# Performance work log

Hardware: AMD Instinct MI355X
Metric: run time of the kernel (lower is better)

## Reference

```python
import jax, jax.numpy as jnp
import numpy as np
from jax import lax

SIGMA = 5
RADIUS = int(4 * SIGMA + 0.5)  # 20 -> kernel size 41, pad_size = 41//2 = 20 = RADIUS
D_AP = 2.27
D_DV = 2.27


def _gauss_d1_kernel():
    # gaussian_kernel1d(sigma, order=1, radius): q(x) = -x/sigma^2, kernel = q(x)*phi(x)
    x = np.arange(-RADIUS, RADIUS + 1).astype(np.float64)
    phi = np.exp(-0.5 / SIGMA ** 2 * x ** 2)
    phi = phi / phi.sum()
    return ((-x / SIGMA ** 2) * phi).astype(np.float32)

_KERNEL = jnp.asarray(_gauss_d1_kernel())


def _conv1d_valid(x, k):
    # x: [N, L], k: [K] -> [N, L-K+1]; cross-correlation, same as torch F.conv1d
    return lax.conv_general_dilated(x[:, None, :], k[None, None, :], (1,), 'VALID')[:, 0, :]


def diffY(x):
    # circular padding along H, derivative / dDV
    c, h, w = x.shape
    xp = jnp.pad(x, ((0, 0), (RADIUS, RADIUS), (0, 0)), mode='wrap')
    xp = jnp.transpose(xp, (0, 2, 1)).reshape(c * w, h + 2 * RADIUS)
    out = _conv1d_valid(xp, _KERNEL).reshape(c, w, h)
    return jnp.transpose(out, (0, 2, 1)) / D_DV


def diffX(x):
    # reflect padding along W, derivative / dAP
    c, h, w = x.shape
    xp = jnp.pad(x, ((0, 0), (0, 0), (RADIUS, RADIUS)), mode='reflect')
    out = _conv1d_valid(xp.reshape(c * h, w + 2 * RADIUS), _KERNEL).reshape(c, h, w)
    return out / D_AP


def setup_inputs() -> dict:
    key = jax.random.key(0)
    k1, k2, k3, k4, k5 = jax.random.split(key, 5)
    H, W = 1024, 2048
    return {
        'y': jax.random.normal(k1, (5, H, W), dtype=jnp.float32),
        'v': jax.random.normal(k2, (2, H, W), dtype=jnp.float32),
        'gamma_ds': jax.random.normal(k3, (H, W), dtype=jnp.float32),
        'cad_coefs': jax.random.uniform(k4, (3,), dtype=jnp.float32),
        'myo_coefs': jax.random.uniform(k5, (5,), dtype=jnp.float32),
    }


def reference(y, v, gamma_ds, cad_coefs, myo_coefs):
    H, W = y.shape[-2:]
    m4 = y[:4]                                  # [4,H,W] myosin components
    c1 = y[4:]                                  # [1,H,W] cadherin

    d1_m = jnp.stack([diffY(m4), diffX(m4)], axis=-1).reshape(2, 2, H, W, 2)
    m = m4.reshape(2, 2, H, W)
    d1_c = jnp.stack([diffY(c1), diffX(c1)], axis=-1).reshape(H, W, 2)
    c = c1[0]

    d1_v = jnp.stack([diffY(v), diffX(v)], axis=-1)   # [2,H,W,2]: d1_v[i,y,x,j] = d_j v_i
    gv = jnp.einsum('iyxj->ijyx', d1_v)
    gvT = jnp.einsum('jyxi->ijyx', d1_v)
    O = -0.5 * (gv - gvT)                       # vorticity
    E = 0.5 * (gv + gvT)                        # strain rate

    eye = jnp.eye(2, dtype=y.dtype)[:, :, None, None]
    trm_yx = jnp.einsum('kkyx->yx', m)
    deviatoric = m - 0.5 * trm_yx[None, None] * eye

    m_norm = jnp.sqrt(jnp.sum(m * m, axis=(0, 1), keepdims=True))            # [1,1,H,W]
    m_0 = jnp.mean(m_norm, axis=(2, 3), keepdims=True)                       # [1,1,1,1]
    dev_mag = jnp.sqrt(jnp.sum(deviatoric * deviatoric, axis=(0, 1), keepdims=True))
    devE = jnp.einsum('klyx,klyx->yx', deviatoric, E)[None, None]

    E_active = E - jnp.sign(devE) * devE * deviatoric / dev_mag ** 2
    E_active = 0.5 * E_active * dev_mag / m_0
    E_passive = E - E_active

    mE = (jnp.einsum('ikyx,kjyx->ijyx', m, E_passive)
          + jnp.einsum('ikyx,kjyx->ijyx', E_passive, m))

    cad = jax.nn.relu(cad_coefs)
    myo = jax.nn.relu(myo_coefs)

    cdot = (-jnp.einsum('iyx,yxi->yx', v, d1_c)
            - cad[0] * c
            + cad[1] * c * jnp.einsum('iyxi->yx', d1_v)
            + cad[2] * gamma_ds)

    trm = trm_yx[None, None]
    gamma_dv = jnp.array([[1.0, 0.0], [0.0, 0.0]], dtype=y.dtype)[:, :, None, None]

    mdot = (-jnp.einsum('kyx,ijyxk->ijyx', v, d1_m)
            - jnp.einsum('ikyx,kjyx->ijyx', O, m)
            + jnp.einsum('ikyx,kjyx->ijyx', m, O)
            - myo[0] * m
            + myo[1] * mE
            - myo[2] * c[None, None] * mE
            + myo[3] * trm * gamma_dv
            + myo[4] * trm * m)

    return jnp.concatenate([mdot.reshape(4, H, W), cdot[None]], axis=0)
```

## Files before the change

kernel.cpp:

```cpp
#include <hip/hip_runtime.h>
#include <math.h>

#define RAD 20
#define KLEN 41
#define NH 1024
#define NW 2048
#define NHW (NH * NW)

struct KW { float w[KLEN]; };
constexpr double cexp_neg(double u) {
  double term = 1.0, sum = 1.0;
  for (int k = 1; k < 30; ++k) { term *= (-u) / (double)k; sum += term; }
  return sum;
}
constexpr KW make_kw() {
  KW r{};
  double ph[KLEN] = {};
  double s = 0.0;
  for (int i = 0; i < KLEN; ++i) {
    double d = (double)(i - RAD);
    double e = cexp_neg(d * d / 800.0);
    e = e * e; e = e * e; e = e * e; e = e * e;
    ph[i] = e; s += e;
  }
  for (int i = 0; i < KLEN; ++i) {
    double d = (double)(i - RAD);
    r.w[i] = (float)((-d / 25.0) * (ph[i] / s) / 2.27);
  }
  return r;
}
static constexpr KW KWC = make_kw();

template <int K>
__device__ __forceinline__ void tap(float s, float& r0, float& r1, float& r2,
                                    float& r3, float& r4, float& r5, float& r6,
                                    float& r7) {
  if constexpr (K - 0 >= 0 && K - 0 <= 40) r0 = fmaf(s, KWC.w[K - 0], r0);
  if constexpr (K - 1 >= 0 && K - 1 <= 40) r1 = fmaf(s, KWC.w[K - 1], r1);
  if constexpr (K - 2 >= 0 && K - 2 <= 40) r2 = fmaf(s, KWC.w[K - 2], r2);
  if constexpr (K - 3 >= 0 && K - 3 <= 40) r3 = fmaf(s, KWC.w[K - 3], r3);
  if constexpr (K - 4 >= 0 && K - 4 <= 40) r4 = fmaf(s, KWC.w[K - 4], r4);
  if constexpr (K - 5 >= 0 && K - 5 <= 40) r5 = fmaf(s, KWC.w[K - 5], r5);
  if constexpr (K - 6 >= 0 && K - 6 <= 40) r6 = fmaf(s, KWC.w[K - 6], r6);
  if constexpr (K - 7 >= 0 && K - 7 <= 40) r7 = fmaf(s, KWC.w[K - 7], r7);
}

#define R8 r0, r1, r2, r3, r4, r5, r6, r7

#define TW 64
#define TH 32
#define TILE_CH ((TH + 2 * RAD) * TW)

__device__ __forceinline__ void conv_col(const float* __restrict__ t, int base,
                                         int lane, float& r0, float& r1,
                                         float& r2, float& r3, float& r4,
                                         float& r5, float& r6, float& r7) {
#define CCHUNK(c)                                      \
  {                                                    \
    float s0 = t[(base + 4 * (c) + 0) * TW + lane];    \
    float s1 = t[(base + 4 * (c) + 1) * TW + lane];    \
    float s2 = t[(base + 4 * (c) + 2) * TW + lane];    \
    float s3 = t[(base + 4 * (c) + 3) * TW + lane];    \
    tap<4 * (c) + 0>(s0, R8);                          \
    tap<4 * (c) + 1>(s1, R8);                          \
    tap<4 * (c) + 2>(s2, R8);                          \
    tap<4 * (c) + 3>(s3, R8);                          \
  }
  CCHUNK(0) CCHUNK(1) CCHUNK(2) CCHUNK(3) CCHUNK(4) CCHUNK(5)
  CCHUNK(6) CCHUNK(7) CCHUNK(8) CCHUNK(9) CCHUNK(10) CCHUNK(11)
#undef CCHUNK
}

__global__ __launch_bounds__(256) void k_reduce(const float* __restrict__ y,
                                                double* __restrict__ acc) {
  const int tid = blockIdx.x * blockDim.x + threadIdx.x;
  const int stride = gridDim.x * blockDim.x;
  double local = 0.0;
  for (int q = tid; q < NHW / 4; q += stride) {
    float4 a = ((const float4*)y)[q];
    float4 b = ((const float4*)(y + NHW))[q];
    float4 c = ((const float4*)(y + 2 * (size_t)NHW))[q];
    float4 d = ((const float4*)(y + 3 * (size_t)NHW))[q];
    local += (double)sqrtf(a.x * a.x + b.x * b.x + c.x * c.x + d.x * d.x);
    local += (double)sqrtf(a.y * a.y + b.y * b.y + c.y * c.y + d.y * d.y);
    local += (double)sqrtf(a.z * a.z + b.z * b.z + c.z * c.z + d.z * d.z);
    local += (double)sqrtf(a.w * a.w + b.w * b.w + c.w * c.w + d.w * d.w);
  }
#pragma unroll
  for (int off = 32; off > 0; off >>= 1) local += __shfl_down(local, off, 64);
  __shared__ double smem[4];
  const int lane = threadIdx.x & 63;
  const int wid = threadIdx.x >> 6;
  if (lane == 0) smem[wid] = local;
  __syncthreads();
  if (threadIdx.x == 0) {
    double s = smem[0] + smem[1] + smem[2] + smem[3];
    atomicAdd(acc, s);
  }
}

__global__ __launch_bounds__(256) void k_dx(const float* __restrict__ y,
                                            const float* __restrict__ v,
                                            float* __restrict__ ws) {
  __shared__ float row[2120];
  const int t = threadIdx.x;
  const int r = blockIdx.x;
  const int ch = blockIdx.y;
  const float* src = (ch < 5) ? (y + (size_t)ch * NHW) : (v + (size_t)(ch - 5) * NHW);
  const float* rp = src + (size_t)r * NW;

#define SWZ(i) ((i) + ((i) >> 6))
#define ST(i, val) { const int ii_ = (i); row[SWZ(ii_)] = (val); }

  const float4* rp4 = (const float4*)rp;
  float4 b0 = rp4[t];
  float4 b1 = rp4[t + 256];
  ST(RAD + 4 * t + 0, b0.x)
  ST(RAD + 4 * t + 1, b0.y)
  ST(RAD + 4 * t + 2, b0.z)
  ST(RAD + 4 * t + 3, b0.w)
  ST(RAD + 4 * (t + 256) + 0, b1.x)
  ST(RAD + 4 * (t + 256) + 1, b1.y)
  ST(RAD + 4 * (t + 256) + 2, b1.z)
  ST(RAD + 4 * (t + 256) + 3, b1.w)
  if (t < RAD) {
    ST(t, rp[RAD - t])
    ST(NW + RAD + t, rp[NW - 2 - t])
  }
  __syncthreads();

  const int xb = 8 * t;
  float r0 = 0.f, r1 = 0.f, r2 = 0.f, r3 = 0.f;
  float r4 = 0.f, r5 = 0.f, r6 = 0.f, r7 = 0.f;
#define RD(k) { const int x_ = xb + (k); float s_ = row[SWZ(x_)]; tap<(k)>(s_, R8); }
  RD(0)  RD(1)  RD(2)  RD(3)  RD(4)  RD(5)  RD(6)  RD(7)
  RD(8)  RD(9)  RD(10) RD(11) RD(12) RD(13) RD(14) RD(15)
  RD(16) RD(17) RD(18) RD(19) RD(20) RD(21) RD(22) RD(23)
  RD(24) RD(25) RD(26) RD(27) RD(28) RD(29) RD(30) RD(31)
  RD(32) RD(33) RD(34) RD(35) RD(36) RD(37) RD(38) RD(39)
  RD(40) RD(41) RD(42) RD(43) RD(44) RD(45) RD(46) RD(47)
#undef RD

  float4 o0, o1;
  o0.x = r0; o0.y = r1; o0.z = r2; o0.w = r3;
  o1.x = r4; o1.y = r5; o1.z = r6; o1.w = r7;
  float4* dst = (float4*)(ws + (size_t)(7 + ch) * NHW + (size_t)r * NW + xb);
  dst[0] = o0;
  dst[1] = o1;
}

__global__ __launch_bounds__(256, 4) void k_dyf(
    const float* __restrict__ y, const float* __restrict__ v,
    const float* __restrict__ gds, const float* __restrict__ cadc,
    const float* __restrict__ myoc, const float* __restrict__ ws,
    const double* __restrict__ acc, float* __restrict__ out) {
  __shared__ float tile[2 * TILE_CH];
  const int lane = threadIdx.x & 63;
  const int wid = threadIdx.x >> 6;
  const int x0 = blockIdx.x * TW;
  const int yb = blockIdx.y * TH;
  const int base = wid * 8;

  const float m0 = (float)(acc[0] / (double)NHW);
  const float cad0 = fmaxf(cadc[0], 0.f);
  const float cad1 = fmaxf(cadc[1], 0.f);
  const float cad2 = fmaxf(cadc[2], 0.f);
  const float my0 = fmaxf(myoc[0], 0.f);
  const float my1 = fmaxf(myoc[1], 0.f);
  const float my2 = fmaxf(myoc[2], 0.f);
  const float my3 = fmaxf(myoc[3], 0.f);
  const float my4 = fmaxf(myoc[4], 0.f);

#define GLL(g, k, srcp)                                                        \
  {                                                                            \
    const float* sp_ = (srcp) +                                                \
        (size_t)(((yb - RAD + wid + 4 * (k)) + NH) & (NH - 1)) * NW + x0 +     \
        lane;                                                                  \
    __builtin_amdgcn_global_load_lds(                                          \
        (const __attribute__((address_space(1))) void*)sp_,                    \
        (__attribute__((address_space(3))) void*)&tile[(g)*TILE_CH +           \
                                                       (wid + 4 * (k)) * TW],  \
        4, 0, 0);                                                              \
  }
#define STAGECH(g, srcp)                                                 \
  GLL(g, 0, srcp) GLL(g, 1, srcp) GLL(g, 2, srcp) GLL(g, 3, srcp)        \
  GLL(g, 4, srcp) GLL(g, 5, srcp) GLL(g, 6, srcp) GLL(g, 7, srcp)        \
  GLL(g, 8, srcp) GLL(g, 9, srcp) GLL(g, 10, srcp) GLL(g, 11, srcp)     \
  GLL(g, 12, srcp) GLL(g, 13, srcp) GLL(g, 14, srcp) GLL(g, 15, srcp)   \
  GLL(g, 16, srcp) GLL(g, 17, srcp)

#define DECL8(P)                                                       \
  float P##0 = 0.f, P##1 = 0.f, P##2 = 0.f, P##3 = 0.f, P##4 = 0.f,    \
        P##5 = 0.f, P##6 = 0.f, P##7 = 0.f;
#define CALLCONV(g, P)                                                  \
  conv_col(&tile[(g) * TILE_CH], base, lane, P##0, P##1, P##2, P##3,    \
           P##4, P##5, P##6, P##7);

  DECL8(ym00) DECL8(ym01) DECL8(ym10) DECL8(ym11)
  DECL8(yc) DECL8(yv0) DECL8(yv1)

  STAGECH(0, y)
  __syncthreads();
  STAGECH(1, y + (size_t)NHW)
  CALLCONV(0, ym00)
  __syncthreads();
  STAGECH(0, y + 2 * (size_t)NHW)
  CALLCONV(1, ym01)
  __syncthreads();
  STAGECH(1, y + 3 * (size_t)NHW)
  CALLCONV(0, ym10)
  __syncthreads();
  STAGECH(0, y + 4 * (size_t)NHW)
  CALLCONV(1, ym11)
  __syncthreads();
  STAGECH(1, v)
  CALLCONV(0, yc)
  __syncthreads();
  STAGECH(0, v + (size_t)NHW)
  CALLCONV(1, yv0)
  __syncthreads();
  CALLCONV(0, yv1)

#define POINT(q)                                                              \
  {                                                                           \
    const size_t idx = (size_t)(yb + base + (q)) * NW + x0 + lane;            \
    const float m00 = y[idx];                                                 \
    const float m01 = y[idx + (size_t)NHW];                                   \
    const float m10 = y[idx + 2 * (size_t)NHW];                               \
    const float m11 = y[idx + 3 * (size_t)NHW];                               \
    const float c = y[idx + 4 * (size_t)NHW];                                 \
    const float v0 = v[idx];                                                  \
    const float v1 = v[idx + (size_t)NHW];                                    \
    const float g = gds[idx];                                                 \
    const float dY_m00 = ym00##q, dY_m01 = ym01##q;                           \
    const float dY_m10 = ym10##q, dY_m11 = ym11##q;                           \
    const float dY_c = yc##q, dY_v0 = yv0##q, dY_v1 = yv1##q;                 \
    const float dX_m00 = ws[idx + 7 * (size_t)NHW];                           \
    const float dX_m01 = ws[idx + 8 * (size_t)NHW];                           \
    const float dX_m10 = ws[idx + 9 * (size_t)NHW];                           \
    const float dX_m11 = ws[idx + 10 * (size_t)NHW];                          \
    const float dX_c = ws[idx + 11 * (size_t)NHW];                            \
    const float dX_v0 = ws[idx + 12 * (size_t)NHW];                           \
    const float dX_v1 = ws[idx + 13 * (size_t)NHW];                           \
    const float gv00 = dY_v0, gv01 = dX_v0, gv10 = dY_v1, gv11 = dX_v1;       \
    const float ww = -0.5f * (gv01 - gv10);                                   \
    const float E00 = gv00, E11 = gv11;                                       \
    const float E01 = 0.5f * (gv01 + gv10);                                   \
    const float E10 = E01;                                                    \
    const float trm = m00 + m11;                                              \
    const float dev00 = m00 - 0.5f * trm;                                     \
    const float dev01 = m01;                                                  \
    const float dev10 = m10;                                                  \
    const float dev11 = m11 - 0.5f * trm;                                     \
    const float dmag_sq =                                                     \
        dev00 * dev00 + dev01 * dev01 + dev10 * dev10 + dev11 * dev11;        \
    const float dm = sqrtf(dmag_sq);                                          \
    const float dm2 = dm * dm;                                                \
    const float devE = dev00 * E00 + dev01 * E01 + dev10 * E10 + dev11 * E11; \
    const float sg = (devE > 0.f) ? 1.f : ((devE < 0.f) ? -1.f : 0.f);        \
    const float coef = sg * devE / dm2;                                       \
    const float sc = 0.5f * dm / m0;                                          \
    const float Ea00 = (E00 - coef * dev00) * sc;                             \
    const float Ea01 = (E01 - coef * dev01) * sc;                             \
    const float Ea10 = (E10 - coef * dev10) * sc;                             \
    const float Ea11 = (E11 - coef * dev11) * sc;                             \
    const float Ep00 = E00 - Ea00;                                            \
    const float Ep01 = E01 - Ea01;                                            \
    const float Ep10 = E10 - Ea10;                                            \
    const float Ep11 = E11 - Ea11;                                            \
    const float mE00 = (m00 * Ep00 + m01 * Ep10) + (Ep00 * m00 + Ep01 * m10); \
    const float mE01 = (m00 * Ep01 + m01 * Ep11) + (Ep00 * m01 + Ep01 * m11); \
    const float mE10 = (m10 * Ep00 + m11 * Ep10) + (Ep10 * m00 + Ep11 * m10); \
    const float mE11 = (m10 * Ep01 + m11 * Ep11) + (Ep10 * m01 + Ep11 * m11); \
    const float divv = gv00 + gv11;                                           \
    const float cdot =                                                        \
        -(v0 * dY_c + v1 * dX_c) - cad0 * c + cad1 * c * divv + cad2 * g;     \
    const float md00 = -(v0 * dY_m00 + v1 * dX_m00) - ww * m10 - ww * m01 -   \
                       my0 * m00 + my1 * mE00 - my2 * c * mE00 + my3 * trm +  \
                       my4 * trm * m00;                                       \
    const float md01 = -(v0 * dY_m01 + v1 * dX_m01) - ww * m11 + ww * m00 -   \
                       my0 * m01 + my1 * mE01 - my2 * c * mE01 +              \
                       my4 * trm * m01;                                       \
    const float md10 = -(v0 * dY_m10 + v1 * dX_m10) + ww * m00 - ww * m11 -   \
                       my0 * m10 + my1 * mE10 - my2 * c * mE10 +              \
                       my4 * trm * m10;                                       \
    const float md11 = -(v0 * dY_m11 + v1 * dX_m11) + ww * m01 + ww * m10 -   \
                       my0 * m11 + my1 * mE11 - my2 * c * mE11 +              \
                       my4 * trm * m11;                                       \
    out[idx] = md00;                                                          \
    out[idx + (size_t)NHW] = md01;                                            \
    out[idx + 2 * (size_t)NHW] = md10;                                        \
    out[idx + 3 * (size_t)NHW] = md11;                                        \
    out[idx + 4 * (size_t)NHW] = cdot;                                        \
  }

  POINT(0) POINT(1) POINT(2) POINT(3)
  POINT(4) POINT(5) POINT(6) POINT(7)
#undef POINT
}

extern "C" void kernel_launch(void* const* d_in, const int* in_sizes, int n_in,
                              void* d_out, int out_size, void* d_ws, size_t ws_size,
                              hipStream_t stream) {
  (void)in_sizes; (void)n_in; (void)out_size; (void)ws_size;
  const float* y = (const float*)d_in[0];
  const float* v = (const float*)d_in[1];
  const float* gds = (const float*)d_in[2];
  const float* cadc = (const float*)d_in[3];
  const float* myoc = (const float*)d_in[4];
  float* out = (float*)d_out;

  double* acc = (double*)d_ws;
  float* planes = (float*)((char*)d_ws + 512);

  hipMemsetAsync(acc, 0, sizeof(double), stream);
  k_reduce<<<dim3(1024), dim3(256), 0, stream>>>(y, acc);
  k_dx<<<dim3(NH, 7), dim3(256), 0, stream>>>(y, v, planes);
  k_dyf<<<dim3(NW / TW, NH / TH), dim3(256), 0, stream>>>(y, v, gds, cadc, myoc,
                                                          planes, acc, out);
}
```

Before: 180.3 us.

## Replace LDS-staged vertical convolution with direct global loads per thread

The Y-direction derivative pass no longer stages 72-row tiles of each channel into shared memory with global_load_lds and barriers. Each thread now reads its 48-row column window straight from global memory and computes 8 outputs per channel, with blocks reshaped to 256 columns by 8 rows. This removes the barriers and LDS traffic but makes each block read a 48-row halo for only 8 output rows, a 6x read amplification that must be served by L2/cache instead of LDS.

```diff
diff --git a/kernel.cpp b/kernel.cpp
--- a/kernel.cpp
+++ b/kernel.cpp
@@ -46,30 +46,6 @@
 }
 
 #define R8 r0, r1, r2, r3, r4, r5, r6, r7
-
-#define TW 64
-#define TH 32
-#define TILE_CH ((TH + 2 * RAD) * TW)
-
-__device__ __forceinline__ void conv_col(const float* __restrict__ t, int base,
-                                         int lane, float& r0, float& r1,
-                                         float& r2, float& r3, float& r4,
-                                         float& r5, float& r6, float& r7) {
-#define CCHUNK(c)                                      \
-  {                                                    \
-    float s0 = t[(base + 4 * (c) + 0) * TW + lane];    \
-    float s1 = t[(base + 4 * (c) + 1) * TW + lane];    \
-    float s2 = t[(base + 4 * (c) + 2) * TW + lane];    \
-    float s3 = t[(base + 4 * (c) + 3) * TW + lane];    \
-    tap<4 * (c) + 0>(s0, R8);                          \
-    tap<4 * (c) + 1>(s1, R8);                          \
-    tap<4 * (c) + 2>(s2, R8);                          \
-    tap<4 * (c) + 3>(s3, R8);                          \
-  }
-  CCHUNK(0) CCHUNK(1) CCHUNK(2) CCHUNK(3) CCHUNK(4) CCHUNK(5)
-  CCHUNK(6) CCHUNK(7) CCHUNK(8) CCHUNK(9) CCHUNK(10) CCHUNK(11)
-#undef CCHUNK
-}
 
 __global__ __launch_bounds__(256) void k_reduce(const float* __restrict__ y,
                                                 double* __restrict__ acc) {
@@ -154,12 +130,8 @@
     const float* __restrict__ gds, const float* __restrict__ cadc,
     const float* __restrict__ myoc, const float* __restrict__ ws,
     const double* __restrict__ acc, float* __restrict__ out) {
-  __shared__ float tile[2 * TILE_CH];
-  const int lane = threadIdx.x & 63;
-  const int wid = threadIdx.x >> 6;
-  const int x0 = blockIdx.x * TW;
-  const int yb = blockIdx.y * TH;
-  const int base = wid * 8;
+  const int x = blockIdx.x * 256 + threadIdx.x;
+  const int yb = blockIdx.y * 8;
 
   const float m0 = (float)(acc[0] / (double)NHW);
   const float cad0 = fmaxf(cadc[0], 0.f);
@@ -171,59 +143,42 @@
   const float my3 = fmaxf(myoc[3], 0.f);
   const float my4 = fmaxf(myoc[4], 0.f);
 
-#define GLL(g, k, srcp)                                                        \
-  {                                                                            \
-    const float* sp_ = (srcp) +                                                \
-        (size_t)(((yb - RAD + wid + 4 * (k)) + NH) & (NH - 1)) * NW + x0 +     \
-        lane;                                                                  \
-    __builtin_amdgcn_global_load_lds(                                          \
-        (const __attribute__((address_space(1))) void*)sp_,                    \
-        (__attribute__((address_space(3))) void*)&tile[(g)*TILE_CH +           \
-                                                       (wid + 4 * (k)) * TW],  \
-        4, 0, 0);                                                              \
-  }
-#define STAGECH(g, srcp)                                                 \
-  GLL(g, 0, srcp) GLL(g, 1, srcp) GLL(g, 2, srcp) GLL(g, 3, srcp)        \
-  GLL(g, 4, srcp) GLL(g, 5, srcp) GLL(g, 6, srcp) GLL(g, 7, srcp)        \
-  GLL(g, 8, srcp) GLL(g, 9, srcp) GLL(g, 10, srcp) GLL(g, 11, srcp)     \
-  GLL(g, 12, srcp) GLL(g, 13, srcp) GLL(g, 14, srcp) GLL(g, 15, srcp)   \
-  GLL(g, 16, srcp) GLL(g, 17, srcp)
-
 #define DECL8(P)                                                       \
   float P##0 = 0.f, P##1 = 0.f, P##2 = 0.f, P##3 = 0.f, P##4 = 0.f,    \
         P##5 = 0.f, P##6 = 0.f, P##7 = 0.f;
-#define CALLCONV(g, P)                                                  \
-  conv_col(&tile[(g) * TILE_CH], base, lane, P##0, P##1, P##2, P##3,    \
-           P##4, P##5, P##6, P##7);
+
+#define CG(P, k)                                                              \
+  {                                                                           \
+    float s_ = sp_[(size_t)(((yb - RAD + (k)) + NH) & (NH - 1)) * NW + x];    \
+    tap<(k)>(s_, P##0, P##1, P##2, P##3, P##4, P##5, P##6, P##7);             \
+  }
+#define CONVG(P, srcp)                                                        \
+  {                                                                           \
+    const float* sp_ = (srcp);                                                \
+    CG(P, 0)  CG(P, 1)  CG(P, 2)  CG(P, 3)  CG(P, 4)  CG(P, 5)               \
+    CG(P, 6)  CG(P, 7)  CG(P, 8)  CG(P, 9)  CG(P, 10) CG(P, 11)              \
+    CG(P, 12) CG(P, 13) CG(P, 14) CG(P, 15) CG(P, 16) CG(P, 17)              \
+    CG(P, 18) CG(P, 19) CG(P, 20) CG(P, 21) CG(P, 22) CG(P, 23)              \
+    CG(P, 24) CG(P, 25) CG(P, 26) CG(P, 27) CG(P, 28) CG(P, 29)              \
+    CG(P, 30) CG(P, 31) CG(P, 32) CG(P, 33) CG(P, 34) CG(P, 35)              \
+    CG(P, 36) CG(P, 37) CG(P, 38) CG(P, 39) CG(P, 40) CG(P, 41)              \
+    CG(P, 42) CG(P, 43) CG(P, 44) CG(P, 45) CG(P, 46) CG(P, 47)              \
+  }
 
   DECL8(ym00) DECL8(ym01) DECL8(ym10) DECL8(ym11)
   DECL8(yc) DECL8(yv0) DECL8(yv1)
 
-  STAGECH(0, y)
-  __syncthreads();
-  STAGECH(1, y + (size_t)NHW)
-  CALLCONV(0, ym00)
-  __syncthreads();
-  STAGECH(0, y + 2 * (size_t)NHW)
-  CALLCONV(1, ym01)
-  __syncthreads();
-  STAGECH(1, y + 3 * (size_t)NHW)
-  CALLCONV(0, ym10)
-  __syncthreads();
-  STAGECH(0, y + 4 * (size_t)NHW)
-  CALLCONV(1, ym11)
-  __syncthreads();
-  STAGECH(1, v)
-  CALLCONV(0, yc)
-  __syncthreads();
-  STAGECH(0, v + (size_t)NHW)
-  CALLCONV(1, yv0)
-  __syncthreads();
-  CALLCONV(0, yv1)
+  CONVG(ym00, y)
+  CONVG(ym01, y + (size_t)NHW)
+  CONVG(ym10, y + 2 * (size_t)NHW)
+  CONVG(ym11, y + 3 * (size_t)NHW)
+  CONVG(yc, y + 4 * (size_t)NHW)
+  CONVG(yv0, v)
+  CONVG(yv1, v + (size_t)NHW)
 
 #define POINT(q)                                                              \
   {                                                                           \
-    const size_t idx = (size_t)(yb + base + (q)) * NW + x0 + lane;            \
+    const size_t idx = (size_t)(yb + (q)) * NW + x;                           \
     const float m00 = y[idx];                                                 \
     const float m01 = y[idx + (size_t)NHW];                                   \
     const float m10 = y[idx + 2 * (size_t)NHW];                               \
@@ -316,6 +271,6 @@
   hipMemsetAsync(acc, 0, sizeof(double), stream);
   k_reduce<<<dim3(1024), dim3(256), 0, stream>>>(y, acc);
   k_dx<<<dim3(NH, 7), dim3(256), 0, stream>>>(y, v, planes);
-  k_dyf<<<dim3(NW / TW, NH / TH), dim3(256), 0, stream>>>(y, v, gds, cadc, myoc,
+  k_dyf<<<dim3(NW / 256, NH / 8), dim3(256), 0, stream>>>(y, v, gds, cadc, myoc,
                                                           planes, acc, out);
 }
```

New measurement: 262.9 us. 45.9% more time.
